# Optimization experiments

Hardware: AMD Instinct MI355X
Metric: run time of the kernel (lower is better)

The kernel has to match this reference:

```python
import jax, jax.numpy as jnp
import numpy as np

N_NODES = 40000
N_EDGES = 640000
IN_CH = 128
HID1, HID2 = 512, 256
OUT_CH = 2
NUM_GRAPHS = 16
EPS = 1e-5


def layer_norm(x, g, b):
    mu = jnp.mean(x, axis=-1, keepdims=True)
    var = jnp.mean(jnp.square(x - mu), axis=-1, keepdims=True)
    return (x - mu) * jax.lax.rsqrt(var + EPS) * g + b


def gcn_conv(x, src, dst, ew, W, b, n_nodes):
    # PyG GCNConv: x' = x @ W; symmetric normalization with self-loops already
    # appended to (src, dst, ew) by the caller; bias added after aggregation.
    xw = x @ W                                            # [N, out]
    deg = jax.ops.segment_sum(ew, dst, num_segments=n_nodes)
    dinv = jnp.where(deg > 0, jax.lax.rsqrt(deg), 0.0)    # deg^{-1/2}, 0 for isolated
    norm = dinv[src] * ew * dinv[dst]                     # [E+N]
    msgs = norm[:, None] * xw[src]                        # gather + scale
    out = jax.ops.segment_sum(msgs, dst, num_segments=n_nodes)
    return out + b


def setup_inputs() -> dict:
    key = jax.random.key(0)
    ks = jax.random.split(key, 12)
    x = jax.random.normal(ks[0], (N_NODES, IN_CH), dtype=jnp.float32)
    edge_index = jax.random.randint(ks[1], (2, N_EDGES), 0, N_NODES, dtype=jnp.int64)
    edge_weight = jax.random.uniform(ks[2], (N_EDGES,), dtype=jnp.float32)
    batch = jnp.sort(jax.random.randint(ks[3], (N_NODES,), 0, NUM_GRAPHS, dtype=jnp.int64))
    # parameters (Glorot-ish scale)
    W1 = jax.random.normal(ks[4], (IN_CH, HID1), dtype=jnp.float32) / np.sqrt(IN_CH)
    b1 = jnp.zeros((HID1,), dtype=jnp.float32)
    g1 = jnp.ones((HID1,), dtype=jnp.float32)
    be1 = jnp.zeros((HID1,), dtype=jnp.float32)
    W2 = jax.random.normal(ks[5], (HID1, HID2), dtype=jnp.float32) / np.sqrt(HID1)
    b2 = jnp.zeros((HID2,), dtype=jnp.float32)
    g2 = jnp.ones((HID2,), dtype=jnp.float32)
    be2 = jnp.zeros((HID2,), dtype=jnp.float32)
    Wfc = jax.random.normal(ks[6], (HID2, OUT_CH), dtype=jnp.float32) / np.sqrt(HID2)
    bfc = jnp.zeros((OUT_CH,), dtype=jnp.float32)
    return {"x": x, "edge_index": edge_index, "edge_weight": edge_weight,
            "batch": batch, "W1": W1, "b1": b1, "g1": g1, "be1": be1,
            "W2": W2, "b2": b2, "g2": g2, "be2": be2, "Wfc": Wfc, "bfc": bfc}


def reference(x, edge_index, edge_weight, batch, W1, b1, g1, be1, W2, b2, g2, be2, Wfc, bfc):
    n = x.shape[0]
    loop = jnp.arange(n, dtype=edge_index.dtype)
    src = jnp.concatenate([edge_index[0], loop])
    dst = jnp.concatenate([edge_index[1], loop])
    ew = jnp.concatenate([edge_weight, jnp.ones((n,), dtype=edge_weight.dtype)])

    h = gcn_conv(x, src, dst, ew, W1, b1, n)
    h = layer_norm(jax.nn.relu(h), g1, be1)          # dropout = identity (eval)
    h3 = gcn_conv(h, src, dst, ew, W2, b2, n)
    h3 = layer_norm(jax.nn.relu(h3), g2, be2)

    # global mean pool over graph ids
    sums = jax.ops.segment_sum(h3, batch, num_segments=NUM_GRAPHS)
    cnts = jax.ops.segment_sum(jnp.ones((n,), dtype=h3.dtype), batch, num_segments=NUM_GRAPHS)
    pooled = sums / jnp.maximum(cnts, 1.0)[:, None]
    out = pooled @ Wfc + bfc
    return h3, out
```

## Files before the change

### kernel.cpp

```cpp
#include <hip/hip_runtime.h>
#include <hip/hip_bf16.h>

#define N_NODES   40000
#define N_EDGES   640000
#define IN_CH     128
#define HID1      512
#define HID2      256
#define OUT_CH    2
#define NUM_GRAPHS 16
#define EPSF      1e-5f
#define SCAN_NB   157

typedef unsigned short u16;
typedef unsigned int   u32;
using short8 = __attribute__((ext_vector_type(8))) short;
using f32x4  = __attribute__((ext_vector_type(4))) float;

__device__ __forceinline__ float b2f(u16 u) {
    return __uint_as_float(((u32)u) << 16);
}
__device__ __forceinline__ u16 f2b(float f) {
    u32 u = __float_as_uint(f);
    u32 r = (u + 0x7FFFu + ((u >> 16) & 1u)) >> 16;
    return (u16)r;
}
__device__ __forceinline__ void gload_lds16(const u16* g, u16* l) {
    __builtin_amdgcn_global_load_lds((const __attribute__((address_space(1))) u32*)g,
                                     (__attribute__((address_space(3))) u32*)l, 16, 0, 0);
}

__global__ __launch_bounds__(256) void degcnt_kernel(const int* __restrict__ dst,
                                                     const float* __restrict__ ew,
                                                     float* __restrict__ deg,
                                                     int* __restrict__ cnt) {
    int t = blockIdx.x * blockDim.x + threadIdx.x;
    if (t < N_EDGES) {
        int d = dst[t];
        atomicAdd(&deg[d], ew[t]);
        atomicAdd(&cnt[d], 1);
    }
}

__global__ __launch_bounds__(256) void dinv_kernel(const float* __restrict__ deg,
                                                   float* __restrict__ dinv) {
    int t = blockIdx.x * blockDim.x + threadIdx.x;
    if (t < N_NODES) dinv[t] = rsqrtf(deg[t] + 1.0f);
}

__global__ __launch_bounds__(256) void scan_p1_kernel(const int* __restrict__ cnt,
                                                      int* __restrict__ rowptr,
                                                      int* __restrict__ blocksum) {
    __shared__ int sd[256];
    const int t = threadIdx.x;
    const int i = blockIdx.x * 256 + t;
    const int v = (i < N_NODES) ? cnt[i] : 0;
    sd[t] = v;
    __syncthreads();
    for (int off = 1; off < 256; off <<= 1) {
        int u = (t >= off) ? sd[t - off] : 0;
        __syncthreads();
        sd[t] += u;
        __syncthreads();
    }
    if (i < N_NODES) rowptr[i] = sd[t] - v;
    if (t == 255) blocksum[blockIdx.x] = sd[255];
}

__global__ __launch_bounds__(256) void scan_p2_kernel(int* __restrict__ blocksum,
                                                      int* __restrict__ bprefix) {
    __shared__ int sd[256];
    const int t = threadIdx.x;
    const int v = (t < SCAN_NB) ? blocksum[t] : 0;
    sd[t] = v;
    __syncthreads();
    for (int off = 1; off < 256; off <<= 1) {
        int u = (t >= off) ? sd[t - off] : 0;
        __syncthreads();
        sd[t] += u;
        __syncthreads();
    }
    bprefix[t] = sd[t] - v;
}

__global__ __launch_bounds__(256) void scan_p3_kernel(int* __restrict__ rowptr,
                                                      const int* __restrict__ bprefix) {
    const int i = blockIdx.x * 256 + threadIdx.x;
    if (i < N_NODES) rowptr[i] += bprefix[blockIdx.x];
    if (i == 0) rowptr[N_NODES] = N_EDGES;
}

__global__ __launch_bounds__(256) void scatter_kernel(const int* __restrict__ src,
                                                      const int* __restrict__ dst,
                                                      const float* __restrict__ ew,
                                                      const float* __restrict__ dinv,
                                                      const int* __restrict__ rowptr,
                                                      int* __restrict__ cursor,
                                                      int* __restrict__ csr_src,
                                                      float* __restrict__ csr_norm) {
    int t = blockIdx.x * blockDim.x + threadIdx.x;
    if (t >= N_EDGES) return;
    int s = src[t], d = dst[t];
    int pos = rowptr[d] + atomicAdd(&cursor[d], 1);
    csr_src[pos] = s;
    csr_norm[pos] = dinv[s] * ew[t] * dinv[d];
}

__global__ __launch_bounds__(256) void cast_x_kernel(const float* __restrict__ x,
                                                     u16* __restrict__ xb) {
    int t = blockIdx.x * blockDim.x + threadIdx.x;
    if (t < N_NODES * IN_CH / 4) {
        float4 v = ((const float4*)x)[t];
        ushort4 o = { f2b(v.x), f2b(v.y), f2b(v.z), f2b(v.w) };
        ((ushort4*)xb)[t] = o;
    }
}

__global__ __launch_bounds__(256) void transpose_cast_kernel(const float* __restrict__ W,
                                                             u16* __restrict__ WT,
                                                             int R, int Ccols) {
    int idx = blockIdx.x * blockDim.x + threadIdx.x;
    if (idx >= R * Ccols) return;
    int r = idx / Ccols, c = idx % Ccols;
    WT[(size_t)c * R + r] = f2b(W[idx]);
}

__global__ __launch_bounds__(256) void agg128_kernel(const int* __restrict__ rowptr,
                                                     const int* __restrict__ csr_src,
                                                     const float* __restrict__ csr_norm,
                                                     const float* __restrict__ dinv,
                                                     const u16* __restrict__ xb,
                                                     u16* __restrict__ outb) {
    const int node = (blockIdx.x * blockDim.x + threadIdx.x) >> 6;
    const int lane = threadIdx.x & 63;
    if (node >= N_NODES) return;
    const float ds = dinv[node];
    const float wself = ds * ds;
    const int e0 = rowptr[node], e1 = rowptr[node + 1];
    const int c0 = lane * 2;

    ushort2 v = *(const ushort2*)&xb[(size_t)node * IN_CH + c0];
    float ax = wself * b2f(v.x), ay = wself * b2f(v.y);
    int e = e0;
    for (; e + 4 <= e1; e += 4) {
        int s0 = csr_src[e], s1 = csr_src[e + 1], s2 = csr_src[e + 2], s3 = csr_src[e + 3];
        float w0 = csr_norm[e], w1 = csr_norm[e + 1], w2 = csr_norm[e + 2], w3 = csr_norm[e + 3];
        ushort2 u0 = *(const ushort2*)&xb[(size_t)s0 * IN_CH + c0];
        ushort2 u1 = *(const ushort2*)&xb[(size_t)s1 * IN_CH + c0];
        ushort2 u2 = *(const ushort2*)&xb[(size_t)s2 * IN_CH + c0];
        ushort2 u3 = *(const ushort2*)&xb[(size_t)s3 * IN_CH + c0];
        ax += w0 * b2f(u0.x) + w1 * b2f(u1.x) + w2 * b2f(u2.x) + w3 * b2f(u3.x);
        ay += w0 * b2f(u0.y) + w1 * b2f(u1.y) + w2 * b2f(u2.y) + w3 * b2f(u3.y);
    }
    for (; e < e1; ++e) {
        int s = csr_src[e];
        float w = csr_norm[e];
        ushort2 u = *(const ushort2*)&xb[(size_t)s * IN_CH + c0];
        ax += w * b2f(u.x);
        ay += w * b2f(u.y);
    }
    ushort2 o = { f2b(ax), f2b(ay) };
    *(ushort2*)&outb[(size_t)node * IN_CH + c0] = o;
}

__global__ __launch_bounds__(256) void agg256_ln_kernel(const int* __restrict__ rowptr,
                                                        const int* __restrict__ csr_src,
                                                        const float* __restrict__ csr_norm,
                                                        const float* __restrict__ dinv,
                                                        const u16* __restrict__ hwb,
                                                        const float* __restrict__ bias,
                                                        const float* __restrict__ g,
                                                        const float* __restrict__ be,
                                                        float* __restrict__ out) {
    const int node = (blockIdx.x * blockDim.x + threadIdx.x) >> 6;
    const int lane = threadIdx.x & 63;
    if (node >= N_NODES) return;
    const float ds = dinv[node];
    const float wself = ds * ds;
    const int e0 = rowptr[node], e1 = rowptr[node + 1];
    const int c0 = lane * 4;

    ushort4 v = *(const ushort4*)&hwb[(size_t)node * HID2 + c0];
    float4 acc = { wself * b2f(v.x), wself * b2f(v.y), wself * b2f(v.z), wself * b2f(v.w) };
    int e = e0;
    for (; e + 4 <= e1; e += 4) {
        int s0 = csr_src[e], s1 = csr_src[e + 1], s2 = csr_src[e + 2], s3 = csr_src[e + 3];
        float w0 = csr_norm[e], w1 = csr_norm[e + 1], w2 = csr_norm[e + 2], w3 = csr_norm[e + 3];
        ushort4 u0 = *(const ushort4*)&hwb[(size_t)s0 * HID2 + c0];
        ushort4 u1 = *(const ushort4*)&hwb[(size_t)s1 * HID2 + c0];
        ushort4 u2 = *(const ushort4*)&hwb[(size_t)s2 * HID2 + c0];
        ushort4 u3 = *(const ushort4*)&hwb[(size_t)s3 * HID2 + c0];
        acc.x += w0 * b2f(u0.x) + w1 * b2f(u1.x) + w2 * b2f(u2.x) + w3 * b2f(u3.x);
        acc.y += w0 * b2f(u0.y) + w1 * b2f(u1.y) + w2 * b2f(u2.y) + w3 * b2f(u3.y);
        acc.z += w0 * b2f(u0.z) + w1 * b2f(u1.z) + w2 * b2f(u2.z) + w3 * b2f(u3.z);
        acc.w += w0 * b2f(u0.w) + w1 * b2f(u1.w) + w2 * b2f(u2.w) + w3 * b2f(u3.w);
    }
    for (; e < e1; ++e) {
        int s = csr_src[e];
        float w = csr_norm[e];
        ushort4 u = *(const ushort4*)&hwb[(size_t)s * HID2 + c0];
        acc.x += w * b2f(u.x);
        acc.y += w * b2f(u.y);
        acc.z += w * b2f(u.z);
        acc.w += w * b2f(u.w);
    }
    float vv[4];
    float sum = 0.f, sq = 0.f;
#pragma unroll
    for (int j = 0; j < 4; ++j) {
        float xv = ((const float*)&acc)[j] + bias[c0 + j];
        xv = fmaxf(xv, 0.f);
        vv[j] = xv;
        sum += xv;
        sq += xv * xv;
    }
#pragma unroll
    for (int off = 32; off >= 1; off >>= 1) {
        sum += __shfl_xor(sum, off);
        sq  += __shfl_xor(sq, off);
    }
    const float mean = sum * (1.0f / HID2);
    const float var = sq * (1.0f / HID2) - mean * mean;
    const float r = rsqrtf(var + EPSF);
    float4 o;
    o.x = (vv[0] - mean) * r * g[c0 + 0] + be[c0 + 0];
    o.y = (vv[1] - mean) * r * g[c0 + 1] + be[c0 + 1];
    o.z = (vv[2] - mean) * r * g[c0 + 2] + be[c0 + 2];
    o.w = (vv[3] - mean) * r * g[c0 + 3] + be[c0 + 3];
    *(float4*)&out[(size_t)node * HID2 + c0] = o;
}

template <int K, int N, int ASTRIDE, bool BF16OUT>
__global__ __launch_bounds__(256) void mfma_gemm128(const u16* __restrict__ A,
                                                    const u16* __restrict__ BT,
                                                    float* __restrict__ Cf,
                                                    u16* __restrict__ Cb) {
    __shared__ u16 As[128 * 32];
    __shared__ u16 Bs[128 * 32];
    const int t = threadIdx.x;
    const int rowbase = blockIdx.x * 128;
    const int colbase = blockIdx.y * 128;
    const int l = t & 63;
    const int wv = t >> 6;
    const int wm = (wv >> 1) * 64;
    const int wn = (wv & 1) * 64;
    const int fr = l & 15;
    const int fg = l >> 4;

    f32x4 acc[4][4];
#pragma unroll
    for (int a = 0; a < 4; ++a)
#pragma unroll
        for (int b = 0; b < 4; ++b)
            acc[a][b] = (f32x4){0.f, 0.f, 0.f, 0.f};

    const int c0i = wv * 128 + l;
    const int c1i = c0i + 64;
    int ar0 = rowbase + (c0i >> 2); if (ar0 >= N_NODES) ar0 = N_NODES - 1;
    int ar1 = rowbase + (c1i >> 2); if (ar1 >= N_NODES) ar1 = N_NODES - 1;
    const u16* ag0 = A + (size_t)ar0 * ASTRIDE + (c0i & 3) * 8;
    const u16* ag1 = A + (size_t)ar1 * ASTRIDE + (c1i & 3) * 8;
    const u16* bg0 = BT + (size_t)(colbase + (c0i >> 2)) * K + (c0i & 3) * 8;
    const u16* bg1 = BT + (size_t)(colbase + (c1i >> 2)) * K + (c1i & 3) * 8;
    u16* al0 = As + c0i * 8;
    u16* al1 = As + c1i * 8;
    u16* bl0 = Bs + c0i * 8;
    u16* bl1 = Bs + c1i * 8;

    for (int k0 = 0; k0 < K; k0 += 32) {
        gload_lds16(ag0 + k0, al0);
        gload_lds16(ag1 + k0, al1);
        gload_lds16(bg0 + k0, bl0);
        gload_lds16(bg1 + k0, bl1);
        __syncthreads();

        short8 af[4], bf[4];
#pragma unroll
        for (int fm = 0; fm < 4; ++fm)
            af[fm] = *(const short8*)&As[(wm + fm * 16 + fr) * 32 + fg * 8];
#pragma unroll
        for (int fn = 0; fn < 4; ++fn)
            bf[fn] = *(const short8*)&Bs[(wn + fn * 16 + fr) * 32 + fg * 8];
#pragma unroll
        for (int fm = 0; fm < 4; ++fm)
#pragma unroll
            for (int fn = 0; fn < 4; ++fn)
                acc[fm][fn] = __builtin_amdgcn_mfma_f32_16x16x32_bf16(af[fm], bf[fn], acc[fm][fn], 0, 0, 0);
        __syncthreads();
    }

#pragma unroll
    for (int fm = 0; fm < 4; ++fm)
#pragma unroll
        for (int fn = 0; fn < 4; ++fn) {
#pragma unroll
            for (int i = 0; i < 4; ++i) {
                int row = rowbase + wm + fm * 16 + fg * 4 + i;
                if (row < N_NODES) {
                    int col = colbase + wn + fn * 16 + fr;
                    if constexpr (BF16OUT)
                        Cb[(size_t)row * N + col] = f2b(acc[fm][fn][i]);
                    else
                        Cf[(size_t)row * N + col] = acc[fm][fn][i];
                }
            }
        }
}

__global__ __launch_bounds__(256) void relu_ln512_kernel(float* __restrict__ io,
                                                         const float* __restrict__ bias,
                                                         const float* __restrict__ g,
                                                         const float* __restrict__ be) {
    const int wv = (blockIdx.x * blockDim.x + threadIdx.x) >> 6;
    const int lane = threadIdx.x & 63;
    if (wv >= N_NODES) return;
    float* __restrict__ row = io + (size_t)wv * HID1;
    float v[8];
    float sum = 0.f, sq = 0.f;
#pragma unroll
    for (int j = 0; j < 8; ++j) {
        int c = lane + 64 * j;
        float x = row[c] + bias[c];
        x = fmaxf(x, 0.f);
        v[j] = x;
        sum += x;
        sq += x * x;
    }
#pragma unroll
    for (int off = 32; off >= 1; off >>= 1) {
        sum += __shfl_xor(sum, off);
        sq  += __shfl_xor(sq, off);
    }
    const float mean = sum * (1.0f / HID1);
    const float var = sq * (1.0f / HID1) - mean * mean;
    const float r = rsqrtf(var + EPSF);
    u16* __restrict__ ob = (u16*)row;
#pragma unroll
    for (int j = 0; j < 8; ++j) {
        int c = lane + 64 * j;
        ob[c] = f2b((v[j] - mean) * r * g[c] + be[c]);
    }
}

__global__ __launch_bounds__(64) void bounds_kernel(const int* __restrict__ batch,
                                                    int* __restrict__ gstart) {
    int g = threadIdx.x;
    if (g > NUM_GRAPHS) return;
    int lo = 0, hi = N_NODES;
    while (lo < hi) {
        int mid = (lo + hi) >> 1;
        if (batch[mid] < g) lo = mid + 1; else hi = mid;
    }
    gstart[g] = lo;
}

__global__ __launch_bounds__(256) void pool2_kernel(const float* __restrict__ h3,
                                                    const int* __restrict__ gstart,
                                                    float* __restrict__ pooled) {
    const int g = blockIdx.x, chunk = blockIdx.y;
    const int s = gstart[g], e = gstart[g + 1];
    const int len = e - s;
    const int c0 = s + (len * chunk) / 16;
    const int c1 = s + (len * (chunk + 1)) / 16;
    float acc = 0.f;
    for (int n = c0; n < c1; ++n)
        acc += h3[(size_t)n * HID2 + threadIdx.x];
    atomicAdd(&pooled[g * HID2 + threadIdx.x], acc);
}

__global__ __launch_bounds__(64) void fc_kernel(const float* __restrict__ pooled,
                                                const int* __restrict__ gstart,
                                                const float* __restrict__ Wfc,
                                                const float* __restrict__ bfc,
                                                float* __restrict__ out) {
    const int t = threadIdx.x;
    if (t >= NUM_GRAPHS * OUT_CH) return;
    const int g = t >> 1;
    const int o = t & 1;
    const int len = gstart[g + 1] - gstart[g];
    const float inv = 1.0f / fmaxf((float)len, 1.0f);
    float s = 0.f;
    for (int k = 0; k < HID2; ++k)
        s += pooled[g * HID2 + k] * Wfc[k * OUT_CH + o];
    out[t] = s * inv + bfc[o];
}

extern "C" void kernel_launch(void* const* d_in, const int* in_sizes, int n_in,
                              void* d_out, int out_size, void* d_ws, size_t ws_size,
                              hipStream_t stream) {
    const float* x   = (const float*)d_in[0];
    const int*   ei  = (const int*)d_in[1];
    const float* ew  = (const float*)d_in[2];
    const int*   bat = (const int*)d_in[3];
    const float* W1  = (const float*)d_in[4];
    const float* b1  = (const float*)d_in[5];
    const float* g1  = (const float*)d_in[6];
    const float* be1 = (const float*)d_in[7];
    const float* W2  = (const float*)d_in[8];
    const float* b2  = (const float*)d_in[9];
    const float* g2  = (const float*)d_in[10];
    const float* be2 = (const float*)d_in[11];
    const float* Wfc = (const float*)d_in[12];
    const float* bfc = (const float*)d_in[13];

    const int* srcArr = ei;
    const int* dstArr = ei + N_EDGES;

    float* out = (float*)d_out;
    float* h3  = out;
    float* fcO = out + (size_t)N_NODES * HID2;

    float* ws       = (float*)d_ws;
    float* deg      = ws;
    int*   cnt      = (int*)(ws + 40960);
    int*   cursor   = (int*)(ws + 81920);
    float* dinv     = ws + 122880;
    int*   rowptr   = (int*)(ws + 163840);
    int*   gstart   = (int*)(ws + 204928);
    int*   blocksum = (int*)(ws + 204992);
    int*   bprefix  = (int*)(ws + 205248);
    int*   csr_src  = (int*)(ws + 205504);
    float* csr_norm = ws + 845504;
    u16*   xb       = (u16*)(ws + 1485504);
    u16*   agg1b    = (u16*)(ws + 4045504);
    float* h_pre    = ws + 6605504;
    u16*   hwb      = (u16*)(ws + 27085504);
    u16*   W1T      = (u16*)(ws + 32205504);
    u16*   W2T      = (u16*)(ws + 32238272);
    float* pooled   = ws + 32303808;

    hipMemsetAsync(deg, 0, 3 * 40960 * sizeof(float), stream);
    degcnt_kernel<<<(N_EDGES + 255) / 256, 256, 0, stream>>>(dstArr, ew, deg, cnt);
    dinv_kernel<<<(N_NODES + 255) / 256, 256, 0, stream>>>(deg, dinv);
    scan_p1_kernel<<<SCAN_NB, 256, 0, stream>>>(cnt, rowptr, blocksum);
    scan_p2_kernel<<<1, 256, 0, stream>>>(blocksum, bprefix);
    scan_p3_kernel<<<SCAN_NB, 256, 0, stream>>>(rowptr, bprefix);
    scatter_kernel<<<(N_EDGES + 255) / 256, 256, 0, stream>>>(
        srcArr, dstArr, ew, dinv, rowptr, cursor, csr_src, csr_norm);

    cast_x_kernel<<<(N_NODES * IN_CH / 4 + 255) / 256, 256, 0, stream>>>(x, xb);
    transpose_cast_kernel<<<(IN_CH * HID1 + 255) / 256, 256, 0, stream>>>(W1, W1T, IN_CH, HID1);
    transpose_cast_kernel<<<(HID1 * HID2 + 255) / 256, 256, 0, stream>>>(W2, W2T, HID1, HID2);

    agg128_kernel<<<(N_NODES + 3) / 4, 256, 0, stream>>>(
        rowptr, csr_src, csr_norm, dinv, xb, agg1b);
    {
        dim3 grid((N_NODES + 127) / 128, HID1 / 128);
        mfma_gemm128<IN_CH, HID1, IN_CH, false><<<grid, 256, 0, stream>>>(
            agg1b, W1T, h_pre, nullptr);
    }
    relu_ln512_kernel<<<(N_NODES + 3) / 4, 256, 0, stream>>>(h_pre, b1, g1, be1);

    {
        dim3 grid((N_NODES + 127) / 128, HID2 / 128);
        mfma_gemm128<HID1, HID2, 1024, true><<<grid, 256, 0, stream>>>(
            (const u16*)h_pre, W2T, nullptr, hwb);
    }
    agg256_ln_kernel<<<(N_NODES + 3) / 4, 256, 0, stream>>>(
        rowptr, csr_src, csr_norm, dinv, hwb, b2, g2, be2, h3);

    bounds_kernel<<<1, 64, 0, stream>>>(bat, gstart);
    hipMemsetAsync(pooled, 0, NUM_GRAPHS * HID2 * sizeof(float), stream);
    {
        dim3 grid(NUM_GRAPHS, 16);
        pool2_kernel<<<grid, 256, 0, stream>>>(h3, gstart, pooled);
    }
    fc_kernel<<<1, 64, 0, stream>>>(pooled, gstart, Wfc, bfc, fcO);
}
```

Measured before the change: 314.9 us.

## Pack degree and count atomics, store GEMM1 output as bf16, unroll aggregation by 8

Replaces the separate float-degree and int-count atomics with a single 64-bit packed atomic that holds a fixed-point degree and an edge count. It records each edge's slot offset so the scatter no longer needs a cursor atomic, and it folds the dinv computation into the scan. GEMM1 now writes bf16 instead of fp32, which halves the traffic of the hidden activation through the ReLU+LN pass and into GEMM2, and the LN kernel uses vectorized 16-byte accesses. The gather loops are unrolled to 8 edges for more memory-level parallelism. The fixed-point degree and the bf16 pre-LN activations add rounding error.

```diff
diff --git a/kernel.cpp b/kernel.cpp
--- a/kernel.cpp
+++ b/kernel.cpp
@@ -10,9 +10,11 @@
 #define NUM_GRAPHS 16
 #define EPSF      1e-5f
 #define SCAN_NB   157
+#define FIXSC     1048576.0f
 
 typedef unsigned short u16;
 typedef unsigned int   u32;
+typedef unsigned long long u64;
 using short8 = __attribute__((ext_vector_type(8))) short;
 using f32x4  = __attribute__((ext_vector_type(4))) float;
 
@@ -29,31 +31,32 @@
                                      (__attribute__((address_space(3))) u32*)l, 16, 0, 0);
 }
 
-__global__ __launch_bounds__(256) void degcnt_kernel(const int* __restrict__ dst,
-                                                     const float* __restrict__ ew,
-                                                     float* __restrict__ deg,
-                                                     int* __restrict__ cnt) {
+__global__ __launch_bounds__(256) void pack_kernel(const int* __restrict__ dst,
+                                                   const float* __restrict__ ew,
+                                                   u64* __restrict__ packed,
+                                                   int* __restrict__ eoff) {
     int t = blockIdx.x * blockDim.x + threadIdx.x;
-    if (t < N_EDGES) {
-        int d = dst[t];
-        atomicAdd(&deg[d], ew[t]);
-        atomicAdd(&cnt[d], 1);
-    }
-}
-
-__global__ __launch_bounds__(256) void dinv_kernel(const float* __restrict__ deg,
-                                                   float* __restrict__ dinv) {
-    int t = blockIdx.x * blockDim.x + threadIdx.x;
-    if (t < N_NODES) dinv[t] = rsqrtf(deg[t] + 1.0f);
-}
-
-__global__ __launch_bounds__(256) void scan_p1_kernel(const int* __restrict__ cnt,
+    if (t >= N_EDGES) return;
+    int d = dst[t];
+    u64 inc = (1ull << 40) | (u64)__float2uint_rn(ew[t] * FIXSC);
+    u64 old = atomicAdd(&packed[d], inc);
+    eoff[t] = (int)(old >> 40);
+}
+
+__global__ __launch_bounds__(256) void scan_p1_kernel(const u64* __restrict__ packed,
+                                                      float* __restrict__ dinv,
                                                       int* __restrict__ rowptr,
                                                       int* __restrict__ blocksum) {
     __shared__ int sd[256];
     const int t = threadIdx.x;
     const int i = blockIdx.x * 256 + t;
-    const int v = (i < N_NODES) ? cnt[i] : 0;
+    int v = 0;
+    if (i < N_NODES) {
+        u64 p = packed[i];
+        v = (int)(p >> 40);
+        float deg = (float)(p & ((1ull << 40) - 1)) * (1.0f / FIXSC);
+        dinv[i] = rsqrtf(deg + 1.0f);
+    }
     sd[t] = v;
     __syncthreads();
     for (int off = 1; off < 256; off <<= 1) {
@@ -94,13 +97,13 @@
                                                       const float* __restrict__ ew,
                                                       const float* __restrict__ dinv,
                                                       const int* __restrict__ rowptr,
-                                                      int* __restrict__ cursor,
+                                                      const int* __restrict__ eoff,
                                                       int* __restrict__ csr_src,
                                                       float* __restrict__ csr_norm) {
     int t = blockIdx.x * blockDim.x + threadIdx.x;
     if (t >= N_EDGES) return;
     int s = src[t], d = dst[t];
-    int pos = rowptr[d] + atomicAdd(&cursor[d], 1);
+    int pos = rowptr[d] + eoff[t];
     csr_src[pos] = s;
     csr_norm[pos] = dinv[s] * ew[t] * dinv[d];
 }
@@ -141,15 +144,17 @@
     ushort2 v = *(const ushort2*)&xb[(size_t)node * IN_CH + c0];
     float ax = wself * b2f(v.x), ay = wself * b2f(v.y);
     int e = e0;
-    for (; e + 4 <= e1; e += 4) {
-        int s0 = csr_src[e], s1 = csr_src[e + 1], s2 = csr_src[e + 2], s3 = csr_src[e + 3];
-        float w0 = csr_norm[e], w1 = csr_norm[e + 1], w2 = csr_norm[e + 2], w3 = csr_norm[e + 3];
-        ushort2 u0 = *(const ushort2*)&xb[(size_t)s0 * IN_CH + c0];
-        ushort2 u1 = *(const ushort2*)&xb[(size_t)s1 * IN_CH + c0];
-        ushort2 u2 = *(const ushort2*)&xb[(size_t)s2 * IN_CH + c0];
-        ushort2 u3 = *(const ushort2*)&xb[(size_t)s3 * IN_CH + c0];
-        ax += w0 * b2f(u0.x) + w1 * b2f(u1.x) + w2 * b2f(u2.x) + w3 * b2f(u3.x);
-        ay += w0 * b2f(u0.y) + w1 * b2f(u1.y) + w2 * b2f(u2.y) + w3 * b2f(u3.y);
+    for (; e + 8 <= e1; e += 8) {
+        int   si[8]; float wi[8]; ushort2 ui[8];
+#pragma unroll
+        for (int j = 0; j < 8; ++j) { si[j] = csr_src[e + j]; wi[j] = csr_norm[e + j]; }
+#pragma unroll
+        for (int j = 0; j < 8; ++j) ui[j] = *(const ushort2*)&xb[(size_t)si[j] * IN_CH + c0];
+#pragma unroll
+        for (int j = 0; j < 8; ++j) {
+            ax += wi[j] * b2f(ui[j].x);
+            ay += wi[j] * b2f(ui[j].y);
+        }
     }
     for (; e < e1; ++e) {
         int s = csr_src[e];
@@ -182,17 +187,19 @@
     ushort4 v = *(const ushort4*)&hwb[(size_t)node * HID2 + c0];
     float4 acc = { wself * b2f(v.x), wself * b2f(v.y), wself * b2f(v.z), wself * b2f(v.w) };
     int e = e0;
-    for (; e + 4 <= e1; e += 4) {
-        int s0 = csr_src[e], s1 = csr_src[e + 1], s2 = csr_src[e + 2], s3 = csr_src[e + 3];
-        float w0 = csr_norm[e], w1 = csr_norm[e + 1], w2 = csr_norm[e + 2], w3 = csr_norm[e + 3];
-        ushort4 u0 = *(const ushort4*)&hwb[(size_t)s0 * HID2 + c0];
-        ushort4 u1 = *(const ushort4*)&hwb[(size_t)s1 * HID2 + c0];
-        ushort4 u2 = *(const ushort4*)&hwb[(size_t)s2 * HID2 + c0];
-        ushort4 u3 = *(const ushort4*)&hwb[(size_t)s3 * HID2 + c0];
-        acc.x += w0 * b2f(u0.x) + w1 * b2f(u1.x) + w2 * b2f(u2.x) + w3 * b2f(u3.x);
-        acc.y += w0 * b2f(u0.y) + w1 * b2f(u1.y) + w2 * b2f(u2.y) + w3 * b2f(u3.y);
-        acc.z += w0 * b2f(u0.z) + w1 * b2f(u1.z) + w2 * b2f(u2.z) + w3 * b2f(u3.z);
-        acc.w += w0 * b2f(u0.w) + w1 * b2f(u1.w) + w2 * b2f(u2.w) + w3 * b2f(u3.w);
+    for (; e + 8 <= e1; e += 8) {
+        int si[8]; float wi[8]; ushort4 ui[8];
+#pragma unroll
+        for (int j = 0; j < 8; ++j) { si[j] = csr_src[e + j]; wi[j] = csr_norm[e + j]; }
+#pragma unroll
+        for (int j = 0; j < 8; ++j) ui[j] = *(const ushort4*)&hwb[(size_t)si[j] * HID2 + c0];
+#pragma unroll
+        for (int j = 0; j < 8; ++j) {
+            acc.x += wi[j] * b2f(ui[j].x);
+            acc.y += wi[j] * b2f(ui[j].y);
+            acc.z += wi[j] * b2f(ui[j].z);
+            acc.w += wi[j] * b2f(ui[j].w);
+        }
     }
     for (; e < e1; ++e) {
         int s = csr_src[e];
@@ -229,10 +236,9 @@
     *(float4*)&out[(size_t)node * HID2 + c0] = o;
 }
 
-template <int K, int N, int ASTRIDE, bool BF16OUT>
+template <int K, int N, int ASTRIDE>
 __global__ __launch_bounds__(256) void mfma_gemm128(const u16* __restrict__ A,
                                                     const u16* __restrict__ BT,
-                                                    float* __restrict__ Cf,
                                                     u16* __restrict__ Cb) {
     __shared__ u16 As[128 * 32];
     __shared__ u16 Bs[128 * 32];
@@ -297,33 +303,31 @@
                 int row = rowbase + wm + fm * 16 + fg * 4 + i;
                 if (row < N_NODES) {
                     int col = colbase + wn + fn * 16 + fr;
-                    if constexpr (BF16OUT)
-                        Cb[(size_t)row * N + col] = f2b(acc[fm][fn][i]);
-                    else
-                        Cf[(size_t)row * N + col] = acc[fm][fn][i];
+                    Cb[(size_t)row * N + col] = f2b(acc[fm][fn][i]);
                 }
             }
         }
 }
 
-__global__ __launch_bounds__(256) void relu_ln512_kernel(float* __restrict__ io,
-                                                         const float* __restrict__ bias,
-                                                         const float* __restrict__ g,
-                                                         const float* __restrict__ be) {
+__global__ __launch_bounds__(256) void relu_ln512b_kernel(u16* __restrict__ io,
+                                                          const float* __restrict__ bias,
+                                                          const float* __restrict__ g,
+                                                          const float* __restrict__ be) {
     const int wv = (blockIdx.x * blockDim.x + threadIdx.x) >> 6;
     const int lane = threadIdx.x & 63;
     if (wv >= N_NODES) return;
-    float* __restrict__ row = io + (size_t)wv * HID1;
+    u16* __restrict__ row = io + (size_t)wv * HID1;
+    const int c0 = lane * 8;
+    short8 raw = *(const short8*)&row[c0];
     float v[8];
     float sum = 0.f, sq = 0.f;
 #pragma unroll
     for (int j = 0; j < 8; ++j) {
-        int c = lane + 64 * j;
-        float x = row[c] + bias[c];
-        x = fmaxf(x, 0.f);
-        v[j] = x;
-        sum += x;
-        sq += x * x;
+        float xv = b2f((u16)raw[j]) + bias[c0 + j];
+        xv = fmaxf(xv, 0.f);
+        v[j] = xv;
+        sum += xv;
+        sq += xv * xv;
     }
 #pragma unroll
     for (int off = 32; off >= 1; off >>= 1) {
@@ -333,12 +337,11 @@
     const float mean = sum * (1.0f / HID1);
     const float var = sq * (1.0f / HID1) - mean * mean;
     const float r = rsqrtf(var + EPSF);
-    u16* __restrict__ ob = (u16*)row;
-#pragma unroll
-    for (int j = 0; j < 8; ++j) {
-        int c = lane + 64 * j;
-        ob[c] = f2b((v[j] - mean) * r * g[c] + be[c]);
-    }
+    short8 o;
+#pragma unroll
+    for (int j = 0; j < 8; ++j)
+        o[j] = (short)f2b((v[j] - mean) * r * g[c0 + j] + be[c0 + j]);
+    *(short8*)&row[c0] = o;
 }
 
 __global__ __launch_bounds__(64) void bounds_kernel(const int* __restrict__ batch,
@@ -410,32 +413,30 @@
     float* fcO = out + (size_t)N_NODES * HID2;
 
     float* ws       = (float*)d_ws;
-    float* deg      = ws;
-    int*   cnt      = (int*)(ws + 40960);
-    int*   cursor   = (int*)(ws + 81920);
-    float* dinv     = ws + 122880;
-    int*   rowptr   = (int*)(ws + 163840);
-    int*   gstart   = (int*)(ws + 204928);
-    int*   blocksum = (int*)(ws + 204992);
-    int*   bprefix  = (int*)(ws + 205248);
-    int*   csr_src  = (int*)(ws + 205504);
-    float* csr_norm = ws + 845504;
-    u16*   xb       = (u16*)(ws + 1485504);
-    u16*   agg1b    = (u16*)(ws + 4045504);
-    float* h_pre    = ws + 6605504;
-    u16*   hwb      = (u16*)(ws + 27085504);
-    u16*   W1T      = (u16*)(ws + 32205504);
-    u16*   W2T      = (u16*)(ws + 32238272);
-    float* pooled   = ws + 32303808;
-
-    hipMemsetAsync(deg, 0, 3 * 40960 * sizeof(float), stream);
-    degcnt_kernel<<<(N_EDGES + 255) / 256, 256, 0, stream>>>(dstArr, ew, deg, cnt);
-    dinv_kernel<<<(N_NODES + 255) / 256, 256, 0, stream>>>(deg, dinv);
-    scan_p1_kernel<<<SCAN_NB, 256, 0, stream>>>(cnt, rowptr, blocksum);
+    u64*   packed   = (u64*)ws;
+    float* dinv     = ws + 81920;
+    int*   rowptr   = (int*)(ws + 122880);
+    int*   gstart   = (int*)(ws + 163968);
+    int*   blocksum = (int*)(ws + 164032);
+    int*   bprefix  = (int*)(ws + 164288);
+    int*   eoff     = (int*)(ws + 164544);
+    int*   csr_src  = (int*)(ws + 804544);
+    float* csr_norm = ws + 1444544;
+    u16*   xb       = (u16*)(ws + 2084544);
+    u16*   agg1b    = (u16*)(ws + 4644544);
+    u16*   hb       = (u16*)(ws + 7204544);
+    u16*   hwb      = (u16*)(ws + 17444544);
+    u16*   W1T      = (u16*)(ws + 22564544);
+    u16*   W2T      = (u16*)(ws + 22597312);
+    float* pooled   = ws + 22662848;
+
+    hipMemsetAsync(packed, 0, 40960 * sizeof(u64), stream);
+    pack_kernel<<<(N_EDGES + 255) / 256, 256, 0, stream>>>(dstArr, ew, packed, eoff);
+    scan_p1_kernel<<<SCAN_NB, 256, 0, stream>>>(packed, dinv, rowptr, blocksum);
     scan_p2_kernel<<<1, 256, 0, stream>>>(blocksum, bprefix);
     scan_p3_kernel<<<SCAN_NB, 256, 0, stream>>>(rowptr, bprefix);
     scatter_kernel<<<(N_EDGES + 255) / 256, 256, 0, stream>>>(
-        srcArr, dstArr, ew, dinv, rowptr, cursor, csr_src, csr_norm);
+        srcArr, dstArr, ew, dinv, rowptr, eoff, csr_src, csr_norm);
 
     cast_x_kernel<<<(N_NODES * IN_CH / 4 + 255) / 256, 256, 0, stream>>>(x, xb);
     transpose_cast_kernel<<<(IN_CH * HID1 + 255) / 256, 256, 0, stream>>>(W1, W1T, IN_CH, HID1);
@@ -445,15 +446,13 @@
         rowptr, csr_src, csr_norm, dinv, xb, agg1b);
     {
         dim3 grid((N_NODES + 127) / 128, HID1 / 128);
-        mfma_gemm128<IN_CH, HID1, IN_CH, false><<<grid, 256, 0, stream>>>(
-            agg1b, W1T, h_pre, nullptr);
-    }
-    relu_ln512_kernel<<<(N_NODES + 3) / 4, 256, 0, stream>>>(h_pre, b1, g1, be1);
+        mfma_gemm128<IN_CH, HID1, IN_CH><<<grid, 256, 0, stream>>>(agg1b, W1T, hb);
+    }
+    relu_ln512b_kernel<<<(N_NODES + 3) / 4, 256, 0, stream>>>(hb, b1, g1, be1);
 
     {
         dim3 grid((N_NODES + 127) / 128, HID2 / 128);
-        mfma_gemm128<HID1, HID2, 1024, true><<<grid, 256, 0, stream>>>(
-            (const u16*)h_pre, W2T, nullptr, hwb);
+        mfma_gemm128<HID1, HID2, HID1><<<grid, 256, 0, stream>>>(hb, W2T, hwb);
     }
     agg256_ln_kernel<<<(N_NODES + 3) / 4, 256, 0, stream>>>(
         rowptr, csr_src, csr_norm, dinv, hwb, b2, g2, be2, h3);
```

After: 270.7 us. 14.0% less time.
